# Kernel tuning notes

Hardware: AMD Instinct MI355X
Metric: run time of the kernel (lower is better)

## Reference

```python
import jax, jax.numpy as jnp
import numpy as np

B, T, D, U = 2048, 200, 128, 128  # batch, history len, input dim, gru units


def setup_inputs() -> dict:
    key = jax.random.key(0)
    ks = jax.random.split(key, 5)
    s = 1.0 / np.sqrt(U + D)
    return {
        "history_state": jax.random.normal(ks[0], (B, T, D), jnp.float32),
        "attention_score": jax.random.uniform(ks[1], (B, T, 1), jnp.float32),
        "Wu": jax.random.normal(ks[2], (U + D, U), jnp.float32) * s,
        "bu": jnp.zeros((U,), jnp.float32),
        "Wr": jax.random.normal(ks[3], (U + D, U), jnp.float32) * s,
        "br": jnp.zeros((U,), jnp.float32),
        "Wh": jax.random.normal(ks[4], (D + U, U), jnp.float32) * s,
        "bh": jnp.zeros((U,), jnp.float32),
    }


def reference(history_state, attention_score, Wu, bu, Wr, br, Wh, bh):
    # time-major for scan: (T, B, ...)
    xs = jnp.swapaxes(history_state, 0, 1)       # (T, B, D)
    ats = jnp.swapaxes(attention_score, 0, 1)    # (T, B, 1)
    h0 = jnp.zeros((history_state.shape[0], Wu.shape[1]), history_state.dtype)

    def step(h, xa):
        x, a = xa
        hx = jnp.concatenate([h, x], axis=-1)                       # (B, U+D)
        u = jax.nn.sigmoid(hx @ Wu + bu)                            # update gate
        r = jax.nn.sigmoid(hx @ Wr + br)                            # reset gate
        hh = jnp.tanh(jnp.concatenate([x, r * h], axis=-1) @ Wh + bh)
        u = u * a                                                   # attention-modulated update
        h_new = u * hh + (1.0 - u) * h
        return h_new, None

    h_final, _ = jax.lax.scan(step, h0, (xs, ats))
    return h_final  # (B, U)
```

## Files before the change

kernel.cpp:

```cpp
#include <hip/hip_runtime.h>
#include <hip/hip_bf16.h>


#define T_LEN 200
#define D_DIM 128
#define U_DIM 128
#define BM    16
#define CH    12
#define NCH   ((T_LEN + CH - 1) / CH)
#define KCS   136
#define XSTEP (16 * KCS)

typedef __attribute__((ext_vector_type(8))) short bf16x8;
typedef __attribute__((ext_vector_type(4))) float f32x4;
typedef __attribute__((ext_vector_type(4))) unsigned int uint4v;

#define MFMA __builtin_amdgcn_mfma_f32_16x16x32_bf16

static __device__ __forceinline__ unsigned short f2bf(float f) {
    unsigned int u = __builtin_bit_cast(unsigned int, f);
    u += 0x7fffu + ((u >> 16) & 1u);
    return (unsigned short)(u >> 16);
}
static __device__ __forceinline__ unsigned int pkbf2(float a, float b) {
    float2 t; t.x = a; t.y = b;
    __hip_bfloat162 v = __float22bfloat162_rn(t);
    unsigned int u; __builtin_memcpy(&u, &v, 4);
    return u;
}
static __device__ __forceinline__ uint4v pack8u(float4 lo, float4 hi) {
    uint4v v;
    v[0] = pkbf2(lo.x, lo.y); v[1] = pkbf2(lo.z, lo.w);
    v[2] = pkbf2(hi.x, hi.y); v[3] = pkbf2(hi.z, hi.w);
    return v;
}
static __device__ __forceinline__ float fast_exp2(float x) {
#if __has_builtin(__builtin_amdgcn_exp2f)
    return __builtin_amdgcn_exp2f(x);
#else
    return exp2f(x);
#endif
}
static __device__ __forceinline__ float fast_rcp(float x) {
#if __has_builtin(__builtin_amdgcn_rcpf)
    return __builtin_amdgcn_rcpf(x);
#else
    return 1.0f / x;
#endif
}
static __device__ __forceinline__ void block_sync_lds() {
    asm volatile("s_waitcnt lgkmcnt(0)" ::: "memory");
    __builtin_amdgcn_sched_barrier(0);
    __builtin_amdgcn_s_barrier();
    __builtin_amdgcn_sched_barrier(0);
}

__global__ __launch_bounds__(512, 1)
void gru_scan_kernel(const float* __restrict__ X,
                     const float* __restrict__ Att,
                     const float* __restrict__ Wu, const float* __restrict__ bu,
                     const float* __restrict__ Wr, const float* __restrict__ br,
                     const float* __restrict__ Wh, const float* __restrict__ bh,
                     float* __restrict__ out)
{
    __shared__ __align__(16) unsigned short x_sm[CH * XSTEP];
    __shared__ __align__(16) unsigned short h_bf[XSTEP];
    __shared__ __align__(16) unsigned short rh_bf[XSTEP];
    __shared__ float a_sm[CH * BM];

    const int tid  = threadIdx.x;
    const int wave = tid >> 6;
    const int lane = tid & 63;
    const int q    = lane >> 4;
    const int ln   = lane & 15;
    const int b0   = blockIdx.x * BM;

    const float INVLN2 = 1.4426950408889634f;

    bf16x8 wu[8], wr[8], wh[8];
    f32x4 nbu, nbr, bh2;
    {
        const int tb = 16 * wave;
        const int c  = tb + ln;
        const f32x4 bu4 = *(const f32x4*)&bu[tb + 4 * q];
        const f32x4 br4 = *(const f32x4*)&br[tb + 4 * q];
        const f32x4 bh4 = *(const f32x4*)&bh[tb + 4 * q];
        #pragma unroll
        for (int r = 0; r < 4; ++r) {
            nbu[r] = -bu4[r] * INVLN2;
            nbr[r] = -br4[r] * INVLN2;
            bh2[r] = 2.0f * bh4[r] * INVLN2;
        }
        #pragma unroll
        for (int kt = 0; kt < 8; ++kt) {
            const int k0 = 32 * kt + 8 * q;
            bf16x8 vu, vr, vh;
            #pragma unroll
            for (int j = 0; j < 8; ++j) {
                vu[j] = (short)f2bf(Wu[(k0 + j) * U_DIM + c] * -INVLN2);
                vr[j] = (short)f2bf(Wr[(k0 + j) * U_DIM + c] * -INVLN2);
                vh[j] = (short)f2bf(Wh[(k0 + j) * U_DIM + c] * (2.0f * INVLN2));
            }
            wu[kt] = vu; wr[kt] = vr; wh[kt] = vh;
        }
    }

    float hreg[4] = {0.f, 0.f, 0.f, 0.f};

    {
        unsigned int* hz = (unsigned int*)h_bf;
        unsigned int* rz = (unsigned int*)rh_bf;
        for (int i = tid; i < XSTEP / 2; i += 512) { hz[i] = 0; rz[i] = 0; }
    }

    const int s2   = tid >> 8;
    const int srow = (tid >> 4) & 15;
    const int cs   = tid & 15;
    const float* xbase = X + (size_t)(b0 + srow) * T_LEN * D_DIM + cs * 8;

    {
        float4 p0[CH];
        #pragma unroll
        for (int w2 = 0; w2 < CH / 2; ++w2) {
            const int t = 2 * w2 + s2;
            const float* src = xbase + (size_t)t * D_DIM;
            p0[2 * w2]     = *(const float4*)(src);
            p0[2 * w2 + 1] = *(const float4*)(src + 4);
        }
        float a_px = 0.0f;
        if (tid < BM * CH)
            a_px = Att[(size_t)(b0 + (tid & 15)) * T_LEN + (tid >> 4)];
        #pragma unroll
        for (int w2 = 0; w2 < CH / 2; ++w2) {
            const int s = 2 * w2 + s2;
            *(uint4v*)&x_sm[s * XSTEP + cs * KCS + srow * 8] =
                pack8u(p0[2 * w2], p0[2 * w2 + 1]);
        }
        if (tid < BM * CH) a_sm[tid] = a_px;
    }
    __syncthreads();

    int t0 = 0;
    for (int ch = 0; ch < NCH; ++ch) {
        const int L  = (t0 + CH <= T_LEN) ? CH : (T_LEN - t0);
        const bool st = (ch + 1 < NCH);

        float4 px[CH];
        float av = 0.0f;
        if (st) {
            const int tn0 = t0 + CH;
            #pragma unroll
            for (int w2 = 0; w2 < CH / 2; ++w2) {
                int t = tn0 + 2 * w2 + s2;
                t = (t < T_LEN) ? t : (T_LEN - 1);
                const float* src = xbase + (size_t)t * D_DIM;
                px[2 * w2]     = *(const float4*)(src);
                px[2 * w2 + 1] = *(const float4*)(src + 4);
            }
            if (tid < BM * CH) {
                int ta = tn0 + (tid >> 4);
                ta = (ta < T_LEN) ? ta : (T_LEN - 1);
                av = Att[(size_t)(b0 + (tid & 15)) * T_LEN + ta];
            }
        }

        f32x4 acc_r, acc_u, acc_h;
        {
            bf16x8 xf[4];
            #pragma unroll
            for (int kt = 0; kt < 4; ++kt)
                xf[kt] = *(const bf16x8*)&x_sm[(4 * kt + q) * KCS + ln * 8];
            acc_r = nbr; acc_u = nbu; acc_h = bh2;
            #pragma unroll
            for (int kt = 0; kt < 4; ++kt) {
                acc_r = MFMA(wr[kt + 4], xf[kt], acc_r, 0, 0, 0);
                acc_u = MFMA(wu[kt + 4], xf[kt], acc_u, 0, 0, 0);
                acc_h = MFMA(wh[kt],     xf[kt], acc_h, 0, 0, 0);
            }
        }

        for (int s = 0; s < L; ++s) {
            bf16x8 hf[4];
            #pragma unroll
            for (int kt = 0; kt < 4; ++kt)
                hf[kt] = *(const bf16x8*)&h_bf[(4 * kt + q) * KCS + ln * 8];
            const float a_att = a_sm[s * BM + ln];

            f32x4 ra = acc_r, rb = (f32x4)0.0f;
            ra = MFMA(wr[0], hf[0], ra, 0, 0, 0);
            rb = MFMA(wr[2], hf[2], rb, 0, 0, 0);
            ra = MFMA(wr[1], hf[1], ra, 0, 0, 0);
            rb = MFMA(wr[3], hf[3], rb, 0, 0, 0);
            #pragma unroll
            for (int kt = 0; kt < 4; ++kt)
                acc_u = MFMA(wu[kt], hf[kt], acc_u, 0, 0, 0);

            {
                float rh[4];
                #pragma unroll
                for (int r = 0; r < 4; ++r) {
                    float zr = ra[r] + rb[r];
                    float rv = fast_rcp(1.0f + fast_exp2(zr));
                    rh[r] = rv * hreg[r];
                }
                uint2 wv; wv.x = pkbf2(rh[0], rh[1]); wv.y = pkbf2(rh[2], rh[3]);
                const int c8 = 2 * wave + (q >> 1);
                *(uint2*)&rh_bf[c8 * KCS + ln * 8 + (q & 1) * 4] = wv;
            }
            block_sync_lds();

            bf16x8 rf[4];
            #pragma unroll
            for (int kt = 0; kt < 4; ++kt)
                rf[kt] = *(const bf16x8*)&rh_bf[(4 * kt + q) * KCS + ln * 8];

            float uq[4];
            #pragma unroll
            for (int r = 0; r < 4; ++r) {
                float u = fast_rcp(1.0f + fast_exp2(acc_u[r]));
                uq[r] = u * a_att;
            }

            f32x4 ha = acc_h, hb = (f32x4)0.0f;
            ha = MFMA(wh[4], rf[0], ha, 0, 0, 0);
            hb = MFMA(wh[6], rf[2], hb, 0, 0, 0);
            ha = MFMA(wh[5], rf[1], ha, 0, 0, 0);
            hb = MFMA(wh[7], rf[3], hb, 0, 0, 0);

            #pragma unroll
            for (int r = 0; r < 4; ++r) {
                float z  = ha[r] + hb[r];
                float hh = 1.0f - 2.0f * fast_rcp(1.0f + fast_exp2(z));
                float ho = hreg[r];
                hreg[r] = ho + uq[r] * (hh - ho);
            }
            {
                uint2 wv; wv.x = pkbf2(hreg[0], hreg[1]); wv.y = pkbf2(hreg[2], hreg[3]);
                const int c8 = 2 * wave + (q >> 1);
                *(uint2*)&h_bf[c8 * KCS + ln * 8 + (q & 1) * 4] = wv;
            }

            if (s + 1 < L) {
                bf16x8 xf[4];
                #pragma unroll
                for (int kt = 0; kt < 4; ++kt)
                    xf[kt] = *(const bf16x8*)&x_sm[(s + 1) * XSTEP + (4 * kt + q) * KCS + ln * 8];
                acc_r = nbr; acc_u = nbu; acc_h = bh2;
                #pragma unroll
                for (int kt = 0; kt < 4; ++kt) {
                    acc_r = MFMA(wr[kt + 4], xf[kt], acc_r, 0, 0, 0);
                    acc_u = MFMA(wu[kt + 4], xf[kt], acc_u, 0, 0, 0);
                    acc_h = MFMA(wh[kt],     xf[kt], acc_h, 0, 0, 0);
                }
            }
            block_sync_lds();
        }

        if (st) {
            #pragma unroll
            for (int w2 = 0; w2 < CH / 2; ++w2) {
                const int s = 2 * w2 + s2;
                *(uint4v*)&x_sm[s * XSTEP + cs * KCS + srow * 8] =
                    pack8u(px[2 * w2], px[2 * w2 + 1]);
            }
            if (tid < BM * CH) a_sm[tid] = av;
            __syncthreads();
        }
        t0 += CH;
    }

    {
        f32x4 v;
        #pragma unroll
        for (int r = 0; r < 4; ++r) v[r] = hreg[r];
        *(f32x4*)&out[(size_t)(b0 + ln) * U_DIM + 16 * wave + 4 * q] = v;
    }
}

extern "C" void kernel_launch(void* const* d_in, const int* in_sizes, int n_in,
                              void* d_out, int out_size, void* d_ws, size_t ws_size,
                              hipStream_t stream) {
    const float* X   = (const float*)d_in[0];
    const float* Att = (const float*)d_in[1];
    const float* Wu  = (const float*)d_in[2];
    const float* bu  = (const float*)d_in[3];
    const float* Wr  = (const float*)d_in[4];
    const float* br  = (const float*)d_in[5];
    const float* Wh  = (const float*)d_in[6];
    const float* bh  = (const float*)d_in[7];
    float* out = (float*)d_out;

    gru_scan_kernel<<<dim3(2048 / BM), dim3(512), 0, stream>>>(
        X, Att, Wu, bu, Wr, br, Wh, bh, out);
}
```

Measured before the change: 452.9 us.

## Interleave next-step input MFMAs with candidate matmul and defer update-gate MFMAs

Result: slower. 466.9 us (+3.1%).

```diff
diff --git a/kernel.cpp b/kernel.cpp
--- a/kernel.cpp
+++ b/kernel.cpp
@@ -180,20 +180,17 @@
         }
 
         for (int s = 0; s < L; ++s) {
+            __builtin_amdgcn_s_setprio(1);
             bf16x8 hf[4];
             #pragma unroll
             for (int kt = 0; kt < 4; ++kt)
                 hf[kt] = *(const bf16x8*)&h_bf[(4 * kt + q) * KCS + ln * 8];
-            const float a_att = a_sm[s * BM + ln];
 
             f32x4 ra = acc_r, rb = (f32x4)0.0f;
             ra = MFMA(wr[0], hf[0], ra, 0, 0, 0);
             rb = MFMA(wr[2], hf[2], rb, 0, 0, 0);
             ra = MFMA(wr[1], hf[1], ra, 0, 0, 0);
             rb = MFMA(wr[3], hf[3], rb, 0, 0, 0);
-            #pragma unroll
-            for (int kt = 0; kt < 4; ++kt)
-                acc_u = MFMA(wu[kt], hf[kt], acc_u, 0, 0, 0);
 
             {
                 float rh[4];
@@ -207,25 +204,55 @@
                 const int c8 = 2 * wave + (q >> 1);
                 *(uint2*)&rh_bf[c8 * KCS + ln * 8 + (q & 1) * 4] = wv;
             }
+            __builtin_amdgcn_s_setprio(0);
             block_sync_lds();
 
+            __builtin_amdgcn_s_setprio(1);
             bf16x8 rf[4];
             #pragma unroll
             for (int kt = 0; kt < 4; ++kt)
                 rf[kt] = *(const bf16x8*)&rh_bf[(4 * kt + q) * KCS + ln * 8];
 
+            #pragma unroll
+            for (int kt = 0; kt < 4; ++kt)
+                acc_u = MFMA(wu[kt], hf[kt], acc_u, 0, 0, 0);
+
+            const bool more = (s + 1 < L);
+            bf16x8 xf[4];
+            if (more) {
+                #pragma unroll
+                for (int kt = 0; kt < 4; ++kt)
+                    xf[kt] = *(const bf16x8*)&x_sm[(s + 1) * XSTEP + (4 * kt + q) * KCS + ln * 8];
+            }
+
+            const float a_att = a_sm[s * BM + ln];
             float uq[4];
             #pragma unroll
-            for (int r = 0; r < 4; ++r) {
-                float u = fast_rcp(1.0f + fast_exp2(acc_u[r]));
-                uq[r] = u * a_att;
-            }
+            for (int r = 0; r < 4; ++r)
+                uq[r] = fast_rcp(1.0f + fast_exp2(acc_u[r])) * a_att;
 
             f32x4 ha = acc_h, hb = (f32x4)0.0f;
             ha = MFMA(wh[4], rf[0], ha, 0, 0, 0);
             hb = MFMA(wh[6], rf[2], hb, 0, 0, 0);
+            if (more) {
+                acc_r = nbr; acc_u = nbu; acc_h = bh2;
+                acc_r = MFMA(wr[4], xf[0], acc_r, 0, 0, 0);
+                acc_u = MFMA(wu[4], xf[0], acc_u, 0, 0, 0);
+                acc_h = MFMA(wh[0], xf[0], acc_h, 0, 0, 0);
+                acc_r = MFMA(wr[5], xf[1], acc_r, 0, 0, 0);
+                acc_u = MFMA(wu[5], xf[1], acc_u, 0, 0, 0);
+                acc_h = MFMA(wh[1], xf[1], acc_h, 0, 0, 0);
+            }
             ha = MFMA(wh[5], rf[1], ha, 0, 0, 0);
             hb = MFMA(wh[7], rf[3], hb, 0, 0, 0);
+            if (more) {
+                acc_r = MFMA(wr[6], xf[2], acc_r, 0, 0, 0);
+                acc_u = MFMA(wu[6], xf[2], acc_u, 0, 0, 0);
+                acc_h = MFMA(wh[2], xf[2], acc_h, 0, 0, 0);
+                acc_r = MFMA(wr[7], xf[3], acc_r, 0, 0, 0);
+                acc_u = MFMA(wu[7], xf[3], acc_u, 0, 0, 0);
+                acc_h = MFMA(wh[3], xf[3], acc_h, 0, 0, 0);
+            }
 
             #pragma unroll
             for (int r = 0; r < 4; ++r) {
@@ -239,20 +266,7 @@
                 const int c8 = 2 * wave + (q >> 1);
                 *(uint2*)&h_bf[c8 * KCS + ln * 8 + (q & 1) * 4] = wv;
             }
-
-            if (s + 1 < L) {
-                bf16x8 xf[4];
-                #pragma unroll
-                for (int kt = 0; kt < 4; ++kt)
-                    xf[kt] = *(const bf16x8*)&x_sm[(s + 1) * XSTEP + (4 * kt + q) * KCS + ln * 8];
-                acc_r = nbr; acc_u = nbu; acc_h = bh2;
-                #pragma unroll
-                for (int kt = 0; kt < 4; ++kt) {
-                    acc_r = MFMA(wr[kt + 4], xf[kt], acc_r, 0, 0, 0);
-                    acc_u = MFMA(wu[kt + 4], xf[kt], acc_u, 0, 0, 0);
-                    acc_h = MFMA(wh[kt],     xf[kt], acc_h, 0, 0, 0);
-                }
-            }
+            __builtin_amdgcn_s_setprio(0);
             block_sync_lds();
         }
 
```
